# Kernel tuning notes

Hardware: AMD Instinct MI355X
Metric: run time of the kernel (lower is better)

Reference implementation:

```python
import jax, jax.numpy as jnp
import numpy as np
from jax import lax

KERNEL = 3
STRIDE = 1
PADDING = 1
DILATION = 1


def setup_inputs() -> dict:
    key = jax.random.key(0)
    k1, k2, k3, k4, k5 = jax.random.split(key, 5)
    B, C, H, W = 8, 64, 256, 256
    x = jax.random.normal(k1, (B, C, H, W), dtype=jnp.float32)
    depthwise_weights = jax.random.normal(k2, (C, 1, KERNEL, KERNEL), dtype=jnp.float32)
    pointwise_weights = jax.random.normal(k3, (C, C, 1, 1), dtype=jnp.float32)
    attention_weights = jax.random.normal(k4, (C, C), dtype=jnp.float32)
    global_attention_weight = jax.random.normal(k5, (C, C), dtype=jnp.float32)
    return {
        "x": x,
        "depthwise_weights": depthwise_weights,
        "pointwise_weights": pointwise_weights,
        "attention_weights": attention_weights,
        "global_attention_weight": global_attention_weight,
    }


def reference(x, depthwise_weights, pointwise_weights, attention_weights, global_attention_weight):
    C = x.shape[1]
    # Depthwise conv: groups == C, NCHW / OIHW layout.
    dw = lax.conv_general_dilated(
        x,
        depthwise_weights,
        window_strides=(STRIDE, STRIDE),
        padding=[(PADDING, PADDING), (PADDING, PADDING)],
        rhs_dilation=(DILATION, DILATION),
        feature_group_count=C,
        dimension_numbers=("NCHW", "OIHW", "NCHW"),
    )  # [B, C, Ho, Wo]
    # Per-pixel channel attention (row-softmax over mixing matrix).
    A = jax.nn.softmax(attention_weights, axis=1)  # [C, C]
    att = jnp.einsum("cd,bdhw->bchw", A, dw)
    # 1x1 pointwise conv (channel mix).
    pw = jnp.einsum("kc,bchw->bkhw", pointwise_weights[:, :, 0, 0], att)
    # Global channel attention.
    G = jax.nn.softmax(global_attention_weight, axis=1)  # [C, C]
    out = jnp.einsum("cd,bdhw->bchw", G, pw)
    return out
```

## Files before the change

### kernel.cpp

```cpp
#include <hip/hip_runtime.h>
#include <math.h>

#define HH 256
#define WW 256
#define CC 64
#define NB 8
#define ROWS 8

typedef float fvec4 __attribute__((ext_vector_type(4)));
typedef float floatx4 __attribute__((ext_vector_type(4)));
typedef _Float16 half8 __attribute__((ext_vector_type(8)));

__global__ __launch_bounds__(1024) void prep_M(const float* __restrict__ A,
                                               const float* __restrict__ G,
                                               const float* __restrict__ P,
                                               _Float16* __restrict__ Mh) {
    __shared__ __align__(16) float As[64][68];
    __shared__ __align__(16) float Gs[64][68];
    __shared__ __align__(16) float T[64][68];

    const int t = threadIdx.x;
    const int wave = t >> 6;
    const int lane = t & 63;

    for (int r8 = 0; r8 < 8; ++r8) {
        int row = wave * 8 + r8;
        int r = row & 63;
        const float* src = (row < 64) ? A : G;
        float v = src[r * 64 + lane];
        float m = v;
        #pragma unroll
        for (int off = 32; off > 0; off >>= 1)
            m = fmaxf(m, __shfl_xor(m, off, 64));
        float e = __expf(v - m);
        float s = e;
        #pragma unroll
        for (int off = 32; off > 0; off >>= 1)
            s += __shfl_xor(s, off, 64);
        float o = e / s;
        if (row < 64) As[r][lane] = o; else Gs[r][lane] = o;
    }
    __syncthreads();

    {
        const int d = t >> 4, q = t & 15;
        float4 acc = make_float4(0.f, 0.f, 0.f, 0.f);
        for (int e = 0; e < 64; ++e) {
            float p = P[d * 64 + e];
            float4 a = *(const float4*)&As[e][4 * q];
            acc.x = fmaf(p, a.x, acc.x);
            acc.y = fmaf(p, a.y, acc.y);
            acc.z = fmaf(p, a.z, acc.z);
            acc.w = fmaf(p, a.w, acc.w);
        }
        *(float4*)&T[d][4 * q] = acc;
    }
    __syncthreads();

    {
        const int k = t >> 4, q = t & 15;
        float4 acc = make_float4(0.f, 0.f, 0.f, 0.f);
        for (int d = 0; d < 64; ++d) {
            float g = Gs[k][d];
            float4 tv = *(const float4*)&T[d][4 * q];
            acc.x = fmaf(g, tv.x, acc.x);
            acc.y = fmaf(g, tv.y, acc.y);
            acc.z = fmaf(g, tv.z, acc.z);
            acc.w = fmaf(g, tv.w, acc.w);
        }
        _Float16* mp = Mh + k * 64 + 4 * q;
        mp[0] = (_Float16)acc.x;
        mp[1] = (_Float16)acc.y;
        mp[2] = (_Float16)acc.z;
        mp[3] = (_Float16)acc.w;
    }
}

__global__ __launch_bounds__(256, 4) void fused_conv_mix(const float* __restrict__ x,
                                                         const float* __restrict__ dwgt,
                                                         const _Float16* __restrict__ Mh,
                                                         float* __restrict__ out) {
    __shared__ __align__(16) float dwT[2][64][68];

    const int t = threadIdx.x;
    const int tw0 = blockIdx.x * 64;
    const int h0 = blockIdx.y * ROWS;
    const int b = blockIdx.z;

    const int c = t >> 2;
    const int chunk = t & 3;
    const int gw0 = tw0 + chunk * 16;
    const float* xc = x + ((size_t)(b * CC + c) * HH) * WW;

    float wg[9];
    #pragma unroll
    for (int i = 0; i < 9; ++i) wg[i] = dwgt[c * 9 + i];

    const int wave = t >> 6;
    const int lane = t & 63;
    const int q = lane >> 4;
    const int mrow = lane & 15;

    half8 af0, af1;
    {
        const half8* ap = (const half8*)(Mh + (wave * 16 + mrow) * 64);
        af0 = ap[q];
        af1 = ap[4 + q];
    }

    float rows[3][18];

    auto load_row = [&](float* r, int y) {
        if ((unsigned)y < (unsigned)HH) {
            const float* p = xc + y * WW + gw0;
            const float4* p4 = (const float4*)p;
            float4 v0 = p4[0], v1 = p4[1], v2 = p4[2], v3 = p4[3];
            r[1] = v0.x;  r[2] = v0.y;  r[3] = v0.z;  r[4] = v0.w;
            r[5] = v1.x;  r[6] = v1.y;  r[7] = v1.z;  r[8] = v1.w;
            r[9] = v2.x;  r[10] = v2.y; r[11] = v2.z; r[12] = v2.w;
            r[13] = v3.x; r[14] = v3.y; r[15] = v3.z; r[16] = v3.w;
            r[0]  = (gw0 > 0)       ? p[-1] : 0.f;
            r[17] = (gw0 + 16 < WW) ? p[16] : 0.f;
        } else {
            #pragma unroll
            for (int i = 0; i < 18; ++i) r[i] = 0.f;
        }
    };

    load_row(rows[0], h0 - 1);
    load_row(rows[1], h0);
    load_row(rows[2], h0 + 1);

    const size_t kstride = (size_t)HH * WW;

    #pragma unroll
    for (int i = 0; i < ROWS; ++i) {
        const float* rm_ = rows[(i + 0) % 3];
        const float* r0_ = rows[(i + 1) % 3];
        const float* rp_ = rows[(i + 2) % 3];

        #pragma unroll
        for (int j = 0; j < 16; ++j) {
            float a = 0.f;
            #pragma unroll
            for (int dx = 0; dx < 3; ++dx) {
                a = fmaf(wg[0 * 3 + dx], rm_[j + dx], a);
                a = fmaf(wg[1 * 3 + dx], r0_[j + dx], a);
                a = fmaf(wg[2 * 3 + dx], rp_[j + dx], a);
            }
            dwT[i & 1][chunk * 16 + j][c] = a;
        }
        __syncthreads();

        if (i < ROWS - 1) load_row(rows[i % 3], h0 + i + 2);

        {
            floatx4 dd[4];
            #pragma unroll
            for (int s = 0; s < 4; ++s) dd[s] = (floatx4){0.f, 0.f, 0.f, 0.f};

            #pragma unroll
            for (int sub = 0; sub < 4; ++sub) {
                const float* bp = &dwT[i & 1][sub * 16 + mrow][q * 8];
                fvec4 alo = *(const fvec4*)(bp);
                fvec4 ahi = *(const fvec4*)(bp + 4);
                fvec4 blo = *(const fvec4*)(bp + 32);
                fvec4 bhi = *(const fvec4*)(bp + 36);
                half8 hb0, hb1;
                #pragma unroll
                for (int j = 0; j < 4; ++j) {
                    hb0[j]     = (_Float16)alo[j];
                    hb0[j + 4] = (_Float16)ahi[j];
                    hb1[j]     = (_Float16)blo[j];
                    hb1[j + 4] = (_Float16)bhi[j];
                }
                dd[sub] = __builtin_amdgcn_mfma_f32_16x16x32_f16(af0, hb0, dd[sub], 0, 0, 0);
                dd[sub] = __builtin_amdgcn_mfma_f32_16x16x32_f16(af1, hb1, dd[sub], 0, 0, 0);
            }

            float* obase = out + (((size_t)(b * CC + wave * 16 + q * 4)) * HH + (h0 + i)) * WW + tw0;
            #pragma unroll
            for (int r = 0; r < 4; ++r) {
                float* orow = obase + (size_t)r * kstride + mrow;
                #pragma unroll
                for (int sub = 0; sub < 4; ++sub)
                    __builtin_nontemporal_store(dd[sub][r], orow + sub * 16);
            }
        }
    }
}

extern "C" void kernel_launch(void* const* d_in, const int* in_sizes, int n_in,
                              void* d_out, int out_size, void* d_ws, size_t ws_size,
                              hipStream_t stream) {
    const float* x    = (const float*)d_in[0];
    const float* dwgt = (const float*)d_in[1];
    const float* pwgt = (const float*)d_in[2];
    const float* attw = (const float*)d_in[3];
    const float* gatt = (const float*)d_in[4];
    _Float16* Mh = (_Float16*)d_ws;
    float* o  = (float*)d_out;

    prep_M<<<1, 1024, 0, stream>>>(attw, gatt, pwgt, Mh);

    dim3 grid(WW / 64, HH / ROWS, NB);
    fused_conv_mix<<<grid, 256, 0, stream>>>(x, dwgt, Mh, o);
}
```

Before: 263.6 us.

## Halve width tile, swap MFMA operands for vectorized float4 stores, raise occupancy

Narrows the spatial tile from 64 to 32 columns, so each thread handles 8 pixels and the grid doubles. The MFMA operands are swapped so the accumulator holds 4 consecutive pixels of one output channel, which allows 16-byte nontemporal vector stores instead of scalar stores. Launch bounds raise the target occupancy from 4 to 7 blocks. In exchange there are more blocks and relatively more halo loads per output pixel.

```diff
diff --git a/kernel.cpp b/kernel.cpp
--- a/kernel.cpp
+++ b/kernel.cpp
@@ -6,6 +6,7 @@
 #define CC 64
 #define NB 8
 #define ROWS 8
+#define TW 32
 
 typedef float fvec4 __attribute__((ext_vector_type(4)));
 typedef float floatx4 __attribute__((ext_vector_type(4)));
@@ -76,20 +77,20 @@
     }
 }
 
-__global__ __launch_bounds__(256, 4) void fused_conv_mix(const float* __restrict__ x,
+__global__ __launch_bounds__(256, 7) void fused_conv_mix(const float* __restrict__ x,
                                                          const float* __restrict__ dwgt,
                                                          const _Float16* __restrict__ Mh,
                                                          float* __restrict__ out) {
-    __shared__ __align__(16) float dwT[2][64][68];
+    __shared__ __align__(16) float dwT[2][TW][68];
 
     const int t = threadIdx.x;
-    const int tw0 = blockIdx.x * 64;
+    const int tw0 = blockIdx.x * TW;
     const int h0 = blockIdx.y * ROWS;
     const int b = blockIdx.z;
 
     const int c = t >> 2;
     const int chunk = t & 3;
-    const int gw0 = tw0 + chunk * 16;
+    const int gw0 = tw0 + chunk * 8;
     const float* xc = x + ((size_t)(b * CC + c) * HH) * WW;
 
     float wg[9];
@@ -108,22 +109,20 @@
         af1 = ap[4 + q];
     }
 
-    float rows[3][18];
+    float rows[3][10];
 
     auto load_row = [&](float* r, int y) {
         if ((unsigned)y < (unsigned)HH) {
             const float* p = xc + y * WW + gw0;
             const float4* p4 = (const float4*)p;
-            float4 v0 = p4[0], v1 = p4[1], v2 = p4[2], v3 = p4[3];
-            r[1] = v0.x;  r[2] = v0.y;  r[3] = v0.z;  r[4] = v0.w;
-            r[5] = v1.x;  r[6] = v1.y;  r[7] = v1.z;  r[8] = v1.w;
-            r[9] = v2.x;  r[10] = v2.y; r[11] = v2.z; r[12] = v2.w;
-            r[13] = v3.x; r[14] = v3.y; r[15] = v3.z; r[16] = v3.w;
-            r[0]  = (gw0 > 0)       ? p[-1] : 0.f;
-            r[17] = (gw0 + 16 < WW) ? p[16] : 0.f;
+            float4 v0 = p4[0], v1 = p4[1];
+            r[1] = v0.x; r[2] = v0.y; r[3] = v0.z; r[4] = v0.w;
+            r[5] = v1.x; r[6] = v1.y; r[7] = v1.z; r[8] = v1.w;
+            r[0] = (gw0 > 0)      ? p[-1] : 0.f;
+            r[9] = (gw0 + 8 < WW) ? p[8]  : 0.f;
         } else {
             #pragma unroll
-            for (int i = 0; i < 18; ++i) r[i] = 0.f;
+            for (int i = 0; i < 10; ++i) r[i] = 0.f;
         }
     };
 
@@ -131,7 +130,7 @@
     load_row(rows[1], h0);
     load_row(rows[2], h0 + 1);
 
-    const size_t kstride = (size_t)HH * WW;
+    float* obase = out + (((size_t)(b * CC + wave * 16 + mrow)) * HH + h0) * WW + tw0 + q * 4;
 
     #pragma unroll
     for (int i = 0; i < ROWS; ++i) {
@@ -140,7 +139,7 @@
         const float* rp_ = rows[(i + 2) % 3];
 
         #pragma unroll
-        for (int j = 0; j < 16; ++j) {
+        for (int j = 0; j < 8; ++j) {
             float a = 0.f;
             #pragma unroll
             for (int dx = 0; dx < 3; ++dx) {
@@ -148,44 +147,54 @@
                 a = fmaf(wg[1 * 3 + dx], r0_[j + dx], a);
                 a = fmaf(wg[2 * 3 + dx], rp_[j + dx], a);
             }
-            dwT[i & 1][chunk * 16 + j][c] = a;
+            dwT[i & 1][chunk * 8 + j][c] = a;
         }
         __syncthreads();
 
         if (i < ROWS - 1) load_row(rows[i % 3], h0 + i + 2);
 
         {
-            floatx4 dd[4];
-            #pragma unroll
-            for (int s = 0; s < 4; ++s) dd[s] = (floatx4){0.f, 0.f, 0.f, 0.f};
-
-            #pragma unroll
-            for (int sub = 0; sub < 4; ++sub) {
-                const float* bp = &dwT[i & 1][sub * 16 + mrow][q * 8];
+            floatx4 dd0 = (floatx4){0.f, 0.f, 0.f, 0.f};
+            floatx4 dd1 = (floatx4){0.f, 0.f, 0.f, 0.f};
+
+            {
+                const float* bp = &dwT[i & 1][mrow][q * 8];
                 fvec4 alo = *(const fvec4*)(bp);
                 fvec4 ahi = *(const fvec4*)(bp + 4);
                 fvec4 blo = *(const fvec4*)(bp + 32);
                 fvec4 bhi = *(const fvec4*)(bp + 36);
-                half8 hb0, hb1;
+                half8 ha, hb;
                 #pragma unroll
                 for (int j = 0; j < 4; ++j) {
-                    hb0[j]     = (_Float16)alo[j];
-                    hb0[j + 4] = (_Float16)ahi[j];
-                    hb1[j]     = (_Float16)blo[j];
-                    hb1[j + 4] = (_Float16)bhi[j];
+                    ha[j]     = (_Float16)alo[j];
+                    ha[j + 4] = (_Float16)ahi[j];
+                    hb[j]     = (_Float16)blo[j];
+                    hb[j + 4] = (_Float16)bhi[j];
                 }
-                dd[sub] = __builtin_amdgcn_mfma_f32_16x16x32_f16(af0, hb0, dd[sub], 0, 0, 0);
-                dd[sub] = __builtin_amdgcn_mfma_f32_16x16x32_f16(af1, hb1, dd[sub], 0, 0, 0);
+                dd0 = __builtin_amdgcn_mfma_f32_16x16x32_f16(ha, af0, dd0, 0, 0, 0);
+                dd0 = __builtin_amdgcn_mfma_f32_16x16x32_f16(hb, af1, dd0, 0, 0, 0);
             }
-
-            float* obase = out + (((size_t)(b * CC + wave * 16 + q * 4)) * HH + (h0 + i)) * WW + tw0;
-            #pragma unroll
-            for (int r = 0; r < 4; ++r) {
-                float* orow = obase + (size_t)r * kstride + mrow;
+            {
+                const float* bp = &dwT[i & 1][16 + mrow][q * 8];
+                fvec4 alo = *(const fvec4*)(bp);
+                fvec4 ahi = *(const fvec4*)(bp + 4);
+                fvec4 blo = *(const fvec4*)(bp + 32);
+                fvec4 bhi = *(const fvec4*)(bp + 36);
+                half8 ha, hb;
                 #pragma unroll
-                for (int sub = 0; sub < 4; ++sub)
-                    __builtin_nontemporal_store(dd[sub][r], orow + sub * 16);
+                for (int j = 0; j < 4; ++j) {
+                    ha[j]     = (_Float16)alo[j];
+                    ha[j + 4] = (_Float16)ahi[j];
+                    hb[j]     = (_Float16)blo[j];
+                    hb[j + 4] = (_Float16)bhi[j];
+                }
+                dd1 = __builtin_amdgcn_mfma_f32_16x16x32_f16(ha, af0, dd1, 0, 0, 0);
+                dd1 = __builtin_amdgcn_mfma_f32_16x16x32_f16(hb, af1, dd1, 0, 0, 0);
             }
+
+            float* op = obase + (size_t)i * WW;
+            __builtin_nontemporal_store(dd0, (floatx4*)op);
+            __builtin_nontemporal_store(dd1, (floatx4*)(op + 16));
         }
     }
 }
@@ -203,6 +212,6 @@
 
     prep_M<<<1, 1024, 0, stream>>>(attw, gatt, pwgt, Mh);
 
-    dim3 grid(WW / 64, HH / ROWS, NB);
+    dim3 grid(WW / TW, HH / ROWS, NB);
     fused_conv_mix<<<grid, 256, 0, stream>>>(x, dwgt, Mh, o);
 }
```

Result: slower. 290.5 us (+10.2%).

## Restructure fused conv-mix: lane-per-pixel loads, shuffle halos, fp16 swizzled LDS, 512 threads

Applied to the files above, without the earlier changes.

Each wave now handles 8 channels, with each lane owning one output column. Global loads become coalesced per channel row, and the horizontal 3-tap neighbours come from wave shuffles plus a small halo fetch instead of overlapping per-thread float4 rows. The LDS staging buffer is stored as fp16 with an XOR swizzle, which removes the per-MFMA fp32-to-fp16 conversion and cuts LDS traffic and bank conflicts. The block grows to 512 threads split across output-channel tiles and pixel halves on a flattened batch-interleaved grid. Depthwise weights are read from global memory inside the loop, and the extra shuffles add instruction overhead.

```diff
diff --git a/kernel.cpp b/kernel.cpp
--- a/kernel.cpp
+++ b/kernel.cpp
@@ -6,8 +6,8 @@
 #define CC 64
 #define NB 8
 #define ROWS 8
-
-typedef float fvec4 __attribute__((ext_vector_type(4)));
+#define TW 64
+
 typedef float floatx4 __attribute__((ext_vector_type(4)));
 typedef _Float16 half8 __attribute__((ext_vector_type(8)));
 
@@ -76,115 +76,125 @@
     }
 }
 
-__global__ __launch_bounds__(256, 4) void fused_conv_mix(const float* __restrict__ x,
+__global__ __launch_bounds__(512, 6) void fused_conv_mix(const float* __restrict__ x,
                                                          const float* __restrict__ dwgt,
                                                          const _Float16* __restrict__ Mh,
                                                          float* __restrict__ out) {
-    __shared__ __align__(16) float dwT[2][64][68];
+    __shared__ _Float16 dwT[2][64][64];
+
+    const int id = blockIdx.x;
+    const int b = id & 7;
+    const int rr = id >> 3;
+    const int tw0 = (rr & 3) * TW;
+    const int h0 = (rr >> 2) * ROWS;
 
     const int t = threadIdx.x;
-    const int tw0 = blockIdx.x * 64;
-    const int h0 = blockIdx.y * ROWS;
-    const int b = blockIdx.z;
-
-    const int c = t >> 2;
-    const int chunk = t & 3;
-    const int gw0 = tw0 + chunk * 16;
-    const float* xc = x + ((size_t)(b * CC + c) * HH) * WW;
-
-    float wg[9];
-    #pragma unroll
-    for (int i = 0; i < 9; ++i) wg[i] = dwgt[c * 9 + i];
-
     const int wave = t >> 6;
     const int lane = t & 63;
+
+    const int c0ch = wave * 8;
+    const float* xb = x + (size_t)b * CC * HH * WW;
+
     const int q = lane >> 4;
     const int mrow = lane & 15;
+    const int ktile = (wave & 3) * 16;
+    const int phalf = (wave >> 2) * 32;
 
     half8 af0, af1;
     {
-        const half8* ap = (const half8*)(Mh + (wave * 16 + mrow) * 64);
+        const half8* ap = (const half8*)(Mh + (ktile + mrow) * 64);
         af0 = ap[q];
         af1 = ap[4 + q];
     }
 
-    float rows[3][18];
-
-    auto load_row = [&](float* r, int y) {
+    float rows_[3][8];
+    float hrow[3];
+
+    auto stage = [&](int s, int y) {
         if ((unsigned)y < (unsigned)HH) {
-            const float* p = xc + y * WW + gw0;
-            const float4* p4 = (const float4*)p;
-            float4 v0 = p4[0], v1 = p4[1], v2 = p4[2], v3 = p4[3];
-            r[1] = v0.x;  r[2] = v0.y;  r[3] = v0.z;  r[4] = v0.w;
-            r[5] = v1.x;  r[6] = v1.y;  r[7] = v1.z;  r[8] = v1.w;
-            r[9] = v2.x;  r[10] = v2.y; r[11] = v2.z; r[12] = v2.w;
-            r[13] = v3.x; r[14] = v3.y; r[15] = v3.z; r[16] = v3.w;
-            r[0]  = (gw0 > 0)       ? p[-1] : 0.f;
-            r[17] = (gw0 + 16 < WW) ? p[16] : 0.f;
+            #pragma unroll
+            for (int cl = 0; cl < 8; ++cl)
+                rows_[s][cl] = xb[((size_t)(c0ch + cl) * HH + y) * WW + tw0 + lane];
+            float hv = 0.f;
+            if (lane < 16) {
+                int cc = c0ch + (lane >> 1);
+                int wq = tw0 - 1 + 65 * (lane & 1);
+                if ((unsigned)wq < (unsigned)WW)
+                    hv = xb[((size_t)cc * HH + y) * WW + wq];
+            }
+            hrow[s] = hv;
         } else {
             #pragma unroll
-            for (int i = 0; i < 18; ++i) r[i] = 0.f;
+            for (int cl = 0; cl < 8; ++cl) rows_[s][cl] = 0.f;
+            hrow[s] = 0.f;
         }
     };
 
-    load_row(rows[0], h0 - 1);
-    load_row(rows[1], h0);
-    load_row(rows[2], h0 + 1);
+    stage(0, h0 - 1);
+    stage(1, h0);
+    stage(2, h0 + 1);
 
     const size_t kstride = (size_t)HH * WW;
+    float* obase = out + (((size_t)(b * CC + ktile + q * 4)) * HH + h0) * WW + tw0 + phalf + mrow;
 
     #pragma unroll
     for (int i = 0; i < ROWS; ++i) {
-        const float* rm_ = rows[(i + 0) % 3];
-        const float* r0_ = rows[(i + 1) % 3];
-        const float* rp_ = rows[(i + 2) % 3];
+        const int sm = (i + 0) % 3;
+        const int s0 = (i + 1) % 3;
+        const int sp = (i + 2) % 3;
 
         #pragma unroll
-        for (int j = 0; j < 16; ++j) {
-            float a = 0.f;
-            #pragma unroll
-            for (int dx = 0; dx < 3; ++dx) {
-                a = fmaf(wg[0 * 3 + dx], rm_[j + dx], a);
-                a = fmaf(wg[1 * 3 + dx], r0_[j + dx], a);
-                a = fmaf(wg[2 * 3 + dx], rp_[j + dx], a);
-            }
-            dwT[i & 1][chunk * 16 + j][c] = a;
+        for (int cl = 0; cl < 8; ++cl) {
+            const int cc = c0ch + cl;
+            const float* wp = dwgt + cc * 9;
+            const float rm = rows_[sm][cl], r0 = rows_[s0][cl], rp = rows_[sp][cl];
+            float cs0 = fmaf(wp[0], rm, fmaf(wp[3], r0, wp[6] * rp));
+            float cs1 = fmaf(wp[1], rm, fmaf(wp[4], r0, wp[7] * rp));
+            float cs2 = fmaf(wp[2], rm, fmaf(wp[5], r0, wp[8] * rp));
+            float lft = __shfl(cs0, lane - 1);
+            float rgt = __shfl(cs2, lane + 1);
+            float bmL = __shfl(hrow[sm], 2 * cl),     b0L = __shfl(hrow[s0], 2 * cl),     bpL = __shfl(hrow[sp], 2 * cl);
+            float bmR = __shfl(hrow[sm], 2 * cl + 1), b0R = __shfl(hrow[s0], 2 * cl + 1), bpR = __shfl(hrow[sp], 2 * cl + 1);
+            float hl = fmaf(wp[0], bmL, fmaf(wp[3], b0L, wp[6] * bpL));
+            float hr = fmaf(wp[2], bmR, fmaf(wp[5], b0R, wp[8] * bpR));
+            lft = (lane == 0) ? hl : lft;
+            rgt = (lane == 63) ? hr : rgt;
+            float o = lft + cs1 + rgt;
+            dwT[i & 1][lane][cc ^ ((lane & 7) << 3)] = (_Float16)o;
         }
         __syncthreads();
 
-        if (i < ROWS - 1) load_row(rows[i % 3], h0 + i + 2);
+        if (i < ROWS - 1) stage(i % 3, h0 + i + 2);
 
         {
-            floatx4 dd[4];
-            #pragma unroll
-            for (int s = 0; s < 4; ++s) dd[s] = (floatx4){0.f, 0.f, 0.f, 0.f};
-
-            #pragma unroll
-            for (int sub = 0; sub < 4; ++sub) {
-                const float* bp = &dwT[i & 1][sub * 16 + mrow][q * 8];
-                fvec4 alo = *(const fvec4*)(bp);
-                fvec4 ahi = *(const fvec4*)(bp + 4);
-                fvec4 blo = *(const fvec4*)(bp + 32);
-                fvec4 bhi = *(const fvec4*)(bp + 36);
-                half8 hb0, hb1;
-                #pragma unroll
-                for (int j = 0; j < 4; ++j) {
-                    hb0[j]     = (_Float16)alo[j];
-                    hb0[j + 4] = (_Float16)ahi[j];
-                    hb1[j]     = (_Float16)blo[j];
-                    hb1[j + 4] = (_Float16)bhi[j];
-                }
-                dd[sub] = __builtin_amdgcn_mfma_f32_16x16x32_f16(af0, hb0, dd[sub], 0, 0, 0);
-                dd[sub] = __builtin_amdgcn_mfma_f32_16x16x32_f16(af1, hb1, dd[sub], 0, 0, 0);
-            }
-
-            float* obase = out + (((size_t)(b * CC + wave * 16 + q * 4)) * HH + (h0 + i)) * WW + tw0;
+            floatx4 dd0 = (floatx4){0.f, 0.f, 0.f, 0.f};
+            floatx4 dd1 = (floatx4){0.f, 0.f, 0.f, 0.f};
+
+            {
+                const int wl = phalf + mrow;
+                const _Float16* bp = &dwT[i & 1][wl][0];
+                const int s8 = (wl & 7) << 3;
+                half8 hb0 = *(const half8*)(bp + ((q * 8) ^ s8));
+                half8 hb1 = *(const half8*)(bp + ((32 + q * 8) ^ s8));
+                dd0 = __builtin_amdgcn_mfma_f32_16x16x32_f16(af0, hb0, dd0, 0, 0, 0);
+                dd0 = __builtin_amdgcn_mfma_f32_16x16x32_f16(af1, hb1, dd0, 0, 0, 0);
+            }
+            {
+                const int wl = phalf + 16 + mrow;
+                const _Float16* bp = &dwT[i & 1][wl][0];
+                const int s8 = (wl & 7) << 3;
+                half8 hb0 = *(const half8*)(bp + ((q * 8) ^ s8));
+                half8 hb1 = *(const half8*)(bp + ((32 + q * 8) ^ s8));
+                dd1 = __builtin_amdgcn_mfma_f32_16x16x32_f16(af0, hb0, dd1, 0, 0, 0);
+                dd1 = __builtin_amdgcn_mfma_f32_16x16x32_f16(af1, hb1, dd1, 0, 0, 0);
+            }
+
+            float* orow = obase + (size_t)i * WW;
             #pragma unroll
             for (int r = 0; r < 4; ++r) {
-                float* orow = obase + (size_t)r * kstride + mrow;
-                #pragma unroll
-                for (int sub = 0; sub < 4; ++sub)
-                    __builtin_nontemporal_store(dd[sub][r], orow + sub * 16);
+                float* op = orow + (size_t)r * kstride;
+                __builtin_nontemporal_store(dd0[r], op);
+                __builtin_nontemporal_store(dd1[r], op + 16);
             }
         }
     }
@@ -203,6 +213,5 @@
 
     prep_M<<<1, 1024, 0, stream>>>(attw, gatt, pwgt, Mh);
 
-    dim3 grid(WW / 64, HH / ROWS, NB);
-    fused_conv_mix<<<grid, 256, 0, stream>>>(x, dwgt, Mh, o);
+    fused_conv_mix<<<dim3(NB * (WW / TW) * (HH / ROWS)), 512, 0, stream>>>(x, dwgt, Mh, o);
 }
```

After: 371.7 us. 41.0% more time.
